# Performance work log

Hardware: AMD Instinct MI355X
Metric: run time of the kernel (lower is better)

Reference implementation:

```python
import jax, jax.numpy as jnp
import numpy as np

NUM_HEADS = 12


def _build_mask(N, unseen_size, dtype):
    # Columns for the last `unseen_size` tokens are masked (-inf) for every
    # query row EXCEPT the diagonal entries in that block (each unseen token
    # may attend to itself). Matches the original Python-loop construction.
    idx = jnp.arange(N)
    col_unseen = idx[None, :] >= (N - unseen_size)
    off_diag = idx[:, None] != idx[None, :]
    return jnp.where(col_unseen & off_diag, -jnp.inf, jnp.asarray(0.0, dtype))


def reference(x, w_qkv, w_proj, b_proj, unseen_size):
    B, N, C = x.shape
    H = NUM_HEADS
    d = C // H
    scale = d ** -0.5
    # qkv: (B,N,3C) -> (3,B,H,N,d)
    qkv = (x @ w_qkv.T).reshape(B, N, 3, H, d).transpose(2, 0, 3, 1, 4)
    q, k, v = qkv[0], qkv[1], qkv[2]
    attn = jnp.einsum('bhqd,bhkd->bhqk', q, k) * scale
    attn = attn + _build_mask(N, unseen_size, attn.dtype)  # broadcast (N,N)
    attn = jax.nn.softmax(attn, axis=-1)
    out = jnp.einsum('bhqk,bhkd->bhqd', attn, v)
    out = out.transpose(0, 2, 1, 3).reshape(B, N, C)
    return out @ w_proj.T + b_proj


def setup_inputs() -> dict:
    key = jax.random.key(0)
    k1, k2, k3 = jax.random.split(key, 3)
    B, N, C = 2, 2048, 768
    x = jax.random.normal(k1, (B, N, C), dtype=jnp.float32)
    w_qkv = jax.random.normal(k2, (3 * C, C), dtype=jnp.float32) * (C ** -0.5)
    w_proj = jax.random.normal(k3, (C, C), dtype=jnp.float32) * (C ** -0.5)
    b_proj = jnp.zeros((C,), dtype=jnp.float32)
    return {"x": x, "w_qkv": w_qkv, "w_proj": w_proj, "b_proj": b_proj,
            "unseen_size": 512}
```

## Files before the change

### kernel.cpp

```cpp
#include <hip/hip_runtime.h>
#include <math.h>

#define NH 12
#define DH 64
#define NSEQ 2048
#define NB 2
#define CDIM 768
#define NVIS 1536

typedef _Float16 half8 __attribute__((ext_vector_type(8)));
typedef _Float16 half4 __attribute__((ext_vector_type(4)));
typedef float floatx4 __attribute__((ext_vector_type(4)));

static constexpr size_t SZ_X    = (size_t)NB*NSEQ*CDIM;
static constexpr size_t SZ_WQKV = (size_t)3*CDIM*CDIM;
static constexpr size_t SZ_WP   = (size_t)CDIM*CDIM;
static constexpr size_t SZ_HEAD = (size_t)NB*NH*NSEQ*DH;

__global__ __launch_bounds__(256) void convert_kernel(
    const float* __restrict__ x, const float* __restrict__ wqkv, const float* __restrict__ wp,
    _Float16* __restrict__ xb, _Float16* __restrict__ wqkvb, _Float16* __restrict__ wpb)
{
  size_t idx = ((size_t)blockIdx.x*256 + threadIdx.x)*4;
  const float* src; _Float16* dst; size_t off;
  if (idx < SZ_X)                        { src = x;    dst = xb;    off = idx; }
  else if (idx < SZ_X+SZ_WQKV)           { src = wqkv; dst = wqkvb; off = idx - SZ_X; }
  else if (idx < SZ_X+SZ_WQKV+SZ_WP)     { src = wp;   dst = wpb;   off = idx - SZ_X - SZ_WQKV; }
  else return;
  float4 v = *reinterpret_cast<const float4*>(src + off);
  _Float16 o[4] = {(_Float16)v.x,(_Float16)v.y,(_Float16)v.z,(_Float16)v.w};
  *reinterpret_cast<uint2*>(dst + off) = *reinterpret_cast<uint2*>(o);
}

template<int MODE>
__global__ __launch_bounds__(256) void gemm_bt(
    const _Float16* __restrict__ A, const _Float16* __restrict__ Bt,
    const float* __restrict__ bias,
    _Float16* __restrict__ qb, _Float16* __restrict__ kb, _Float16* __restrict__ vb,
    float* __restrict__ outp)
{
  constexpr int K = CDIM;
  constexpr int LDSST = 40;
  __shared__ _Float16 As[128*LDSST];
  __shared__ _Float16 Bs[128*LDSST];
  const int tid = threadIdx.x;
  const int lane = tid & 63, wid = tid >> 6;
  const int l15 = lane & 15, quad = lane >> 4;
  const int wm = (wid >> 1)*64, wn = (wid & 1)*64;
  const int tileN = blockIdx.x*128, tileM = blockIdx.y*128;
  const int srow = tid >> 2, scol = (tid & 3)*8;
  floatx4 acc[4][4] = {};
  for (int k0 = 0; k0 < K; k0 += 32) {
    uint4 a0 = *reinterpret_cast<const uint4*>(A  + (size_t)(tileM+srow)*K    + k0 + scol);
    uint4 a1 = *reinterpret_cast<const uint4*>(A  + (size_t)(tileM+64+srow)*K + k0 + scol);
    uint4 b0 = *reinterpret_cast<const uint4*>(Bt + (size_t)(tileN+srow)*K    + k0 + scol);
    uint4 b1 = *reinterpret_cast<const uint4*>(Bt + (size_t)(tileN+64+srow)*K + k0 + scol);
    __syncthreads();
    *reinterpret_cast<uint4*>(&As[srow*LDSST + scol])      = a0;
    *reinterpret_cast<uint4*>(&As[(64+srow)*LDSST + scol]) = a1;
    *reinterpret_cast<uint4*>(&Bs[srow*LDSST + scol])      = b0;
    *reinterpret_cast<uint4*>(&Bs[(64+srow)*LDSST + scol]) = b1;
    __syncthreads();
    half8 af[4], bfr[4];
    #pragma unroll
    for (int mi=0; mi<4; mi++)
      af[mi] = *reinterpret_cast<const half8*>(&As[(wm+mi*16+l15)*LDSST + quad*8]);
    #pragma unroll
    for (int ni=0; ni<4; ni++)
      bfr[ni] = *reinterpret_cast<const half8*>(&Bs[(wn+ni*16+l15)*LDSST + quad*8]);
    #pragma unroll
    for (int mi=0; mi<4; mi++)
      #pragma unroll
      for (int ni=0; ni<4; ni++)
        acc[mi][ni] = __builtin_amdgcn_mfma_f32_16x16x32_f16(af[mi], bfr[ni], acc[mi][ni], 0,0,0);
  }
  #pragma unroll
  for (int mi=0; mi<4; mi++)
    #pragma unroll
    for (int ni=0; ni<4; ni++) {
      int n = tileN + wn + ni*16 + l15;
      int m0 = tileM + wm + mi*16 + quad*4;
      if (MODE == 0) {
        int part = n / CDIM, rem = n - part*CDIM;
        int h = rem >> 6, dd = rem & 63;
        int b = m0 >> 11, i0 = m0 & 2047;
        if (part == 2) {
          half4 pk = {(_Float16)acc[mi][ni][0], (_Float16)acc[mi][ni][1],
                      (_Float16)acc[mi][ni][2], (_Float16)acc[mi][ni][3]};
          *reinterpret_cast<half4*>(&vb[(((size_t)b*NH + h)*DH + dd)*NSEQ + i0]) = pk;
        } else {
          _Float16* dst = part ? kb : qb;
          float sc = part ? 1.0f : 0.125f*1.44269504f;
          #pragma unroll
          for (int r = 0; r < 4; r++)
            dst[(((size_t)b*NH + h)*NSEQ + i0 + r)*DH + dd] = (_Float16)(acc[mi][ni][r]*sc);
        }
      } else {
        #pragma unroll
        for (int r = 0; r < 4; r++)
          outp[(size_t)(m0 + r)*CDIM + n] = acc[mi][ni][r] + bias[n];
      }
    }
}

__global__ __launch_bounds__(256, 3) void fa_kernel(
    const _Float16* __restrict__ qg, const _Float16* __restrict__ kg,
    const _Float16* __restrict__ vtg, _Float16* __restrict__ og)
{
  constexpr int LDP = 72;
  __shared__ _Float16 Ps[64*LDP];
  __shared__ float Ls[4*64];
  const int blk = blockIdx.x;
  const int idx = blk >> 3;
  const int bh = (blk & 7)*3 + (idx % 3);
  const int qbase = (idx / 3) * 64;
  const int tid = threadIdx.x;
  const int lane = tid & 63, w = tid >> 6;
  const int l15 = lane & 15, quad = lane >> 4;
  const _Float16* qp  = qg  + (size_t)bh*NSEQ*DH;
  const _Float16* kbp = kg  + (size_t)bh*NSEQ*DH;
  const _Float16* vbp = vtg + (size_t)bh*DH*NSEQ;
  half8 qf[4][2];
  #pragma unroll
  for (int g = 0; g < 4; g++)
    #pragma unroll
    for (int c = 0; c < 2; c++)
      qf[g][c] = *reinterpret_cast<const half8*>(qp + (size_t)(qbase + g*16 + l15)*DH + c*32 + quad*8);
  const _Float16* kRow = kbp + (size_t)(w*16 + l15)*DH + quad*8;
  const _Float16* vRow = vbp + (size_t)(w*16 + l15)*NSEQ + quad*8;
  half8 kc0 = *reinterpret_cast<const half8*>(kRow);
  half8 kc1 = *reinterpret_cast<const half8*>(kRow + 32);
  half8 vc0 = *reinterpret_cast<const half8*>(vRow);
  half8 vc1 = *reinterpret_cast<const half8*>(vRow + 32);
  floatx4 o[4] = {};
  float lsum[4] = {0.f, 0.f, 0.f, 0.f};
  for (int t = 0; t < 24; t++) {
    const int tn = (t + 1 < 24) ? t + 1 : 0;
    half8 kn0 = *reinterpret_cast<const half8*>(kRow + (size_t)tn*64*DH);
    half8 kn1 = *reinterpret_cast<const half8*>(kRow + (size_t)tn*64*DH + 32);
    half8 vn0 = *reinterpret_cast<const half8*>(vRow + tn*64);
    half8 vn1 = *reinterpret_cast<const half8*>(vRow + tn*64 + 32);
    floatx4 st[4] = {};
    #pragma unroll
    for (int g = 0; g < 4; g++) {
      st[g] = __builtin_amdgcn_mfma_f32_16x16x32_f16(kc0, qf[g][0], st[g], 0,0,0);
      st[g] = __builtin_amdgcn_mfma_f32_16x16x32_f16(kc1, qf[g][1], st[g], 0,0,0);
    }
    half4 pk[4];
    #pragma unroll
    for (int g = 0; g < 4; g++) {
      float e0 = exp2f(st[g][0]), e1 = exp2f(st[g][1]);
      float e2 = exp2f(st[g][2]), e3 = exp2f(st[g][3]);
      lsum[g] += (e0+e1)+(e2+e3);
      pk[g] = half4{(_Float16)e0,(_Float16)e1,(_Float16)e2,(_Float16)e3};
    }
    __syncthreads();
    #pragma unroll
    for (int g = 0; g < 4; g++)
      *reinterpret_cast<half4*>(&Ps[(g*16+l15)*LDP + w*16 + quad*4]) = pk[g];
    __syncthreads();
    #pragma unroll
    for (int g = 0; g < 4; g++) {
      half8 pb0 = *reinterpret_cast<const half8*>(&Ps[(g*16+l15)*LDP + quad*8]);
      half8 pb1 = *reinterpret_cast<const half8*>(&Ps[(g*16+l15)*LDP + 32 + quad*8]);
      o[g] = __builtin_amdgcn_mfma_f32_16x16x32_f16(vc0, pb0, o[g], 0,0,0);
      o[g] = __builtin_amdgcn_mfma_f32_16x16x32_f16(vc1, pb1, o[g], 0,0,0);
    }
    kc0 = kn0; kc1 = kn1; vc0 = vn0; vc1 = vn1;
  }
  #pragma unroll
  for (int g = 0; g < 4; g++) {
    lsum[g] += __shfl_xor(lsum[g], 16);
    lsum[g] += __shfl_xor(lsum[g], 32);
  }
  if (lane < 16) {
    #pragma unroll
    for (int g = 0; g < 4; g++) Ls[w*64 + g*16 + lane] = lsum[g];
  }
  __syncthreads();
  float den[4];
  #pragma unroll
  for (int g = 0; g < 4; g++)
    den[g] = Ls[g*16+l15] + Ls[64+g*16+l15] + Ls[128+g*16+l15] + Ls[192+g*16+l15];
  if (qbase >= NVIS) {
    #pragma unroll
    for (int g = 0; g < 4; g++) {
      half8 kd0 = *reinterpret_cast<const half8*>(kbp + (size_t)(qbase + g*16 + l15)*DH + quad*8);
      half8 kd1 = *reinterpret_cast<const half8*>(kbp + (size_t)(qbase + g*16 + l15)*DH + 32 + quad*8);
      float pd = 0.f;
      #pragma unroll
      for (int j = 0; j < 8; j++)
        pd += (float)qf[g][0][j]*(float)kd0[j] + (float)qf[g][1][j]*(float)kd1[j];
      pd += __shfl_xor(pd, 16);
      pd += __shfl_xor(pd, 32);
      float e = exp2f(pd);
      den[g] += e;
      #pragma unroll
      for (int r = 0; r < 4; r++)
        o[g][r] += e * (float)vbp[(size_t)(w*16+quad*4+r)*NSEQ + qbase + g*16 + l15];
    }
  }
  const int b = bh / NH, h = bh - b*NH;
  #pragma unroll
  for (int g = 0; g < 4; g++) {
    float inv = 1.0f / den[g];
    half4 pk = {(_Float16)(o[g][0]*inv), (_Float16)(o[g][1]*inv),
                (_Float16)(o[g][2]*inv), (_Float16)(o[g][3]*inv)};
    size_t oaddr = ((size_t)b*NSEQ + qbase + g*16 + l15)*CDIM + h*DH + w*16 + quad*4;
    *reinterpret_cast<half4*>(&og[oaddr]) = pk;
  }
}

extern "C" void kernel_launch(void* const* d_in, const int* in_sizes, int n_in,
                              void* d_out, int out_size, void* d_ws, size_t ws_size,
                              hipStream_t stream) {
  (void)in_sizes; (void)n_in; (void)out_size; (void)ws_size;
  const float* x     = (const float*)d_in[0];
  const float* wqkv  = (const float*)d_in[1];
  const float* wproj = (const float*)d_in[2];
  const float* bproj = (const float*)d_in[3];

  _Float16* xb    = (_Float16*)d_ws;
  _Float16* wqkvb = xb + SZ_X;
  _Float16* wpb   = wqkvb + SZ_WQKV;
  _Float16* qb    = wpb + SZ_WP;
  _Float16* kb    = qb + SZ_HEAD;
  _Float16* vb    = kb + SZ_HEAD;
  _Float16* ob    = vb + SZ_HEAD;
  float* outp = (float*)d_out;

  size_t total = SZ_X + SZ_WQKV + SZ_WP;
  int cblocks = (int)((total/4 + 255)/256);
  convert_kernel<<<cblocks, 256, 0, stream>>>(x, wqkv, wproj, xb, wqkvb, wpb);
  gemm_bt<0><<<dim3(3*CDIM/128, NB*NSEQ/128), 256, 0, stream>>>(xb, wqkvb, nullptr, qb, kb, vb, nullptr);
  fa_kernel<<<NB*NH*(NSEQ/64), 256, 0, stream>>>(qb, kb, vb, ob);
  gemm_bt<1><<<dim3(CDIM/128, NB*NSEQ/128), 256, 0, stream>>>(ob, wpb, bproj, nullptr, nullptr, nullptr, outp);
}
```

Before: 176.4 us.

## Use direct global-to-LDS loads with swizzle in GEMM, widen attention KV tile

The GEMM now stages A/B tiles with global_load_lds (direct global-to-LDS DMA) into an XOR-swizzled unpadded layout instead of going through registers. The projection GEMM gets a narrower 64-column tile so more blocks are launched. The attention kernel processes 128 keys per iteration instead of 64, which halves the number of barrier pairs and doubles the register prefetch depth for K and V. It also swaps exp2f for the builtin exp2. Risks include higher register pressure in the attention kernel and correctness depending on the swizzle matching the LDS write pattern.

```diff
diff --git a/kernel.cpp b/kernel.cpp
--- a/kernel.cpp
+++ b/kernel.cpp
@@ -16,6 +16,10 @@
 static constexpr size_t SZ_WQKV = (size_t)3*CDIM*CDIM;
 static constexpr size_t SZ_WP   = (size_t)CDIM*CDIM;
 static constexpr size_t SZ_HEAD = (size_t)NB*NH*NSEQ*DH;
+
+#define GLOAD_LDS16(gp, lp) \
+  __builtin_amdgcn_global_load_lds((const __attribute__((address_space(1))) void*)(gp), \
+                                   (__attribute__((address_space(3))) void*)(lp), 16, 0, 0)
 
 __global__ __launch_bounds__(256) void convert_kernel(
     const float* __restrict__ x, const float* __restrict__ wqkv, const float* __restrict__ wp,
@@ -32,7 +36,7 @@
   *reinterpret_cast<uint2*>(dst + off) = *reinterpret_cast<uint2*>(o);
 }
 
-template<int MODE>
+template<int MODE, int BN>
 __global__ __launch_bounds__(256) void gemm_bt(
     const _Float16* __restrict__ A, const _Float16* __restrict__ Bt,
     const float* __restrict__ bias,
@@ -40,44 +44,53 @@
     float* __restrict__ outp)
 {
   constexpr int K = CDIM;
-  constexpr int LDSST = 40;
-  __shared__ _Float16 As[128*LDSST];
-  __shared__ _Float16 Bs[128*LDSST];
+  constexpr int BM = 128, BK = 32;
+  constexpr int MI = (BN == 128) ? 4 : 2;
+  constexpr int NI = 4;
+  __shared__ _Float16 As[BM*BK];
+  __shared__ _Float16 Bs[BN*BK];
   const int tid = threadIdx.x;
   const int lane = tid & 63, wid = tid >> 6;
   const int l15 = lane & 15, quad = lane >> 4;
-  const int wm = (wid >> 1)*64, wn = (wid & 1)*64;
-  const int tileN = blockIdx.x*128, tileM = blockIdx.y*128;
-  const int srow = tid >> 2, scol = (tid & 3)*8;
-  floatx4 acc[4][4] = {};
-  for (int k0 = 0; k0 < K; k0 += 32) {
-    uint4 a0 = *reinterpret_cast<const uint4*>(A  + (size_t)(tileM+srow)*K    + k0 + scol);
-    uint4 a1 = *reinterpret_cast<const uint4*>(A  + (size_t)(tileM+64+srow)*K + k0 + scol);
-    uint4 b0 = *reinterpret_cast<const uint4*>(Bt + (size_t)(tileN+srow)*K    + k0 + scol);
-    uint4 b1 = *reinterpret_cast<const uint4*>(Bt + (size_t)(tileN+64+srow)*K + k0 + scol);
-    __syncthreads();
-    *reinterpret_cast<uint4*>(&As[srow*LDSST + scol])      = a0;
-    *reinterpret_cast<uint4*>(&As[(64+srow)*LDSST + scol]) = a1;
-    *reinterpret_cast<uint4*>(&Bs[srow*LDSST + scol])      = b0;
-    *reinterpret_cast<uint4*>(&Bs[(64+srow)*LDSST + scol]) = b1;
-    __syncthreads();
-    half8 af[4], bfr[4];
-    #pragma unroll
-    for (int mi=0; mi<4; mi++)
-      af[mi] = *reinterpret_cast<const half8*>(&As[(wm+mi*16+l15)*LDSST + quad*8]);
-    #pragma unroll
-    for (int ni=0; ni<4; ni++)
-      bfr[ni] = *reinterpret_cast<const half8*>(&Bs[(wn+ni*16+l15)*LDSST + quad*8]);
-    #pragma unroll
-    for (int mi=0; mi<4; mi++)
-      #pragma unroll
-      for (int ni=0; ni<4; ni++)
+  const int wm = (BN == 128) ? (wid >> 1)*64 : wid*32;
+  const int wn = (BN == 128) ? (wid & 1)*64 : 0;
+  const int tileN = blockIdx.x*BN, tileM = blockIdx.y*BM;
+  const int lrow = lane >> 2, lchunk = lane & 3;
+  const int gcol = ((lchunk ^ (lrow >> 1)) & 3)*8;
+  const _Float16* gA0 = A  + (size_t)(tileM + wid*32      + lrow)*K + gcol;
+  const _Float16* gA1 = A  + (size_t)(tileM + wid*32 + 16 + lrow)*K + gcol;
+  const _Float16* gB0 = Bt + (size_t)(tileN + ((BN==128) ? wid*32 : wid*16) + lrow)*K + gcol;
+  const _Float16* gB1 = Bt + (size_t)(tileN + wid*32 + 16 + lrow)*K + gcol;
+  _Float16* lA0 = As + (wid*32)*BK;
+  _Float16* lA1 = As + (wid*32 + 16)*BK;
+  _Float16* lB0 = Bs + ((BN==128) ? wid*32 : wid*16)*BK;
+  _Float16* lB1 = Bs + (wid*32 + 16)*BK;
+  const int cp = ((quad ^ (l15 >> 1)) & 3)*8;
+  floatx4 acc[MI][NI] = {};
+  for (int k0 = 0; k0 < K; k0 += BK) {
+    __syncthreads();
+    GLOAD_LDS16(gA0 + k0, lA0);
+    GLOAD_LDS16(gA1 + k0, lA1);
+    GLOAD_LDS16(gB0 + k0, lB0);
+    if (BN == 128) GLOAD_LDS16(gB1 + k0, lB1);
+    __syncthreads();
+    half8 af[MI], bfr[NI];
+    #pragma unroll
+    for (int mi = 0; mi < MI; mi++)
+      af[mi] = *reinterpret_cast<const half8*>(&As[(wm + mi*16 + l15)*BK + cp]);
+    #pragma unroll
+    for (int ni = 0; ni < NI; ni++)
+      bfr[ni] = *reinterpret_cast<const half8*>(&Bs[(wn + ni*16 + l15)*BK + cp]);
+    #pragma unroll
+    for (int mi = 0; mi < MI; mi++)
+      #pragma unroll
+      for (int ni = 0; ni < NI; ni++)
         acc[mi][ni] = __builtin_amdgcn_mfma_f32_16x16x32_f16(af[mi], bfr[ni], acc[mi][ni], 0,0,0);
   }
   #pragma unroll
-  for (int mi=0; mi<4; mi++)
-    #pragma unroll
-    for (int ni=0; ni<4; ni++) {
+  for (int mi = 0; mi < MI; mi++)
+    #pragma unroll
+    for (int ni = 0; ni < NI; ni++) {
       int n = tileN + wn + ni*16 + l15;
       int m0 = tileM + wm + mi*16 + quad*4;
       if (MODE == 0) {
@@ -107,7 +120,7 @@
     const _Float16* __restrict__ qg, const _Float16* __restrict__ kg,
     const _Float16* __restrict__ vtg, _Float16* __restrict__ og)
 {
-  constexpr int LDP = 72;
+  constexpr int LDP = 136;
   __shared__ _Float16 Ps[64*LDP];
   __shared__ float Ls[4*64];
   const int blk = blockIdx.x;
@@ -128,45 +141,64 @@
       qf[g][c] = *reinterpret_cast<const half8*>(qp + (size_t)(qbase + g*16 + l15)*DH + c*32 + quad*8);
   const _Float16* kRow = kbp + (size_t)(w*16 + l15)*DH + quad*8;
   const _Float16* vRow = vbp + (size_t)(w*16 + l15)*NSEQ + quad*8;
-  half8 kc0 = *reinterpret_cast<const half8*>(kRow);
-  half8 kc1 = *reinterpret_cast<const half8*>(kRow + 32);
-  half8 vc0 = *reinterpret_cast<const half8*>(vRow);
-  half8 vc1 = *reinterpret_cast<const half8*>(vRow + 32);
+  half8 kc[2][2], vc[2][2];
+  #pragma unroll
+  for (int s = 0; s < 2; s++)
+    #pragma unroll
+    for (int c = 0; c < 2; c++) {
+      kc[s][c] = *reinterpret_cast<const half8*>(kRow + (size_t)(s*64)*DH + c*32);
+      vc[s][c] = *reinterpret_cast<const half8*>(vRow + s*64 + c*32);
+    }
   floatx4 o[4] = {};
   float lsum[4] = {0.f, 0.f, 0.f, 0.f};
-  for (int t = 0; t < 24; t++) {
-    const int tn = (t + 1 < 24) ? t + 1 : 0;
-    half8 kn0 = *reinterpret_cast<const half8*>(kRow + (size_t)tn*64*DH);
-    half8 kn1 = *reinterpret_cast<const half8*>(kRow + (size_t)tn*64*DH + 32);
-    half8 vn0 = *reinterpret_cast<const half8*>(vRow + tn*64);
-    half8 vn1 = *reinterpret_cast<const half8*>(vRow + tn*64 + 32);
-    floatx4 st[4] = {};
+  for (int t = 0; t < 12; t++) {
+    const int tn = (t + 1 < 12) ? t + 1 : 0;
+    half8 kn[2][2], vn[2][2];
+    #pragma unroll
+    for (int s = 0; s < 2; s++)
+      #pragma unroll
+      for (int c = 0; c < 2; c++) {
+        kn[s][c] = *reinterpret_cast<const half8*>(kRow + (size_t)(tn*128 + s*64)*DH + c*32);
+        vn[s][c] = *reinterpret_cast<const half8*>(vRow + tn*128 + s*64 + c*32);
+      }
+    half4 pk[2][4];
+    #pragma unroll
+    for (int s = 0; s < 2; s++) {
+      floatx4 st[4] = {};
+      #pragma unroll
+      for (int g = 0; g < 4; g++) {
+        st[g] = __builtin_amdgcn_mfma_f32_16x16x32_f16(kc[s][0], qf[g][0], st[g], 0,0,0);
+        st[g] = __builtin_amdgcn_mfma_f32_16x16x32_f16(kc[s][1], qf[g][1], st[g], 0,0,0);
+      }
+      #pragma unroll
+      for (int g = 0; g < 4; g++) {
+        float e0 = __builtin_exp2f(st[g][0]), e1 = __builtin_exp2f(st[g][1]);
+        float e2 = __builtin_exp2f(st[g][2]), e3 = __builtin_exp2f(st[g][3]);
+        lsum[g] += (e0+e1)+(e2+e3);
+        pk[s][g] = half4{(_Float16)e0,(_Float16)e1,(_Float16)e2,(_Float16)e3};
+      }
+    }
+    __syncthreads();
+    #pragma unroll
+    for (int s = 0; s < 2; s++)
+      #pragma unroll
+      for (int g = 0; g < 4; g++)
+        *reinterpret_cast<half4*>(&Ps[(g*16+l15)*LDP + s*64 + w*16 + quad*4]) = pk[s][g];
+    __syncthreads();
     #pragma unroll
     for (int g = 0; g < 4; g++) {
-      st[g] = __builtin_amdgcn_mfma_f32_16x16x32_f16(kc0, qf[g][0], st[g], 0,0,0);
-      st[g] = __builtin_amdgcn_mfma_f32_16x16x32_f16(kc1, qf[g][1], st[g], 0,0,0);
-    }
-    half4 pk[4];
-    #pragma unroll
-    for (int g = 0; g < 4; g++) {
-      float e0 = exp2f(st[g][0]), e1 = exp2f(st[g][1]);
-      float e2 = exp2f(st[g][2]), e3 = exp2f(st[g][3]);
-      lsum[g] += (e0+e1)+(e2+e3);
-      pk[g] = half4{(_Float16)e0,(_Float16)e1,(_Float16)e2,(_Float16)e3};
-    }
-    __syncthreads();
-    #pragma unroll
-    for (int g = 0; g < 4; g++)
-      *reinterpret_cast<half4*>(&Ps[(g*16+l15)*LDP + w*16 + quad*4]) = pk[g];
-    __syncthreads();
-    #pragma unroll
-    for (int g = 0; g < 4; g++) {
-      half8 pb0 = *reinterpret_cast<const half8*>(&Ps[(g*16+l15)*LDP + quad*8]);
-      half8 pb1 = *reinterpret_cast<const half8*>(&Ps[(g*16+l15)*LDP + 32 + quad*8]);
-      o[g] = __builtin_amdgcn_mfma_f32_16x16x32_f16(vc0, pb0, o[g], 0,0,0);
-      o[g] = __builtin_amdgcn_mfma_f32_16x16x32_f16(vc1, pb1, o[g], 0,0,0);
-    }
-    kc0 = kn0; kc1 = kn1; vc0 = vn0; vc1 = vn1;
+      #pragma unroll
+      for (int s = 0; s < 2; s++)
+        #pragma unroll
+        for (int c = 0; c < 2; c++) {
+          half8 pb = *reinterpret_cast<const half8*>(&Ps[(g*16+l15)*LDP + s*64 + c*32 + quad*8]);
+          o[g] = __builtin_amdgcn_mfma_f32_16x16x32_f16(vc[s][c], pb, o[g], 0,0,0);
+        }
+    }
+    #pragma unroll
+    for (int s = 0; s < 2; s++)
+      #pragma unroll
+      for (int c = 0; c < 2; c++) { kc[s][c] = kn[s][c]; vc[s][c] = vn[s][c]; }
   }
   #pragma unroll
   for (int g = 0; g < 4; g++) {
@@ -193,7 +225,7 @@
         pd += (float)qf[g][0][j]*(float)kd0[j] + (float)qf[g][1][j]*(float)kd1[j];
       pd += __shfl_xor(pd, 16);
       pd += __shfl_xor(pd, 32);
-      float e = exp2f(pd);
+      float e = __builtin_exp2f(pd);
       den[g] += e;
       #pragma unroll
       for (int r = 0; r < 4; r++)
@@ -232,7 +264,7 @@
   size_t total = SZ_X + SZ_WQKV + SZ_WP;
   int cblocks = (int)((total/4 + 255)/256);
   convert_kernel<<<cblocks, 256, 0, stream>>>(x, wqkv, wproj, xb, wqkvb, wpb);
-  gemm_bt<0><<<dim3(3*CDIM/128, NB*NSEQ/128), 256, 0, stream>>>(xb, wqkvb, nullptr, qb, kb, vb, nullptr);
+  gemm_bt<0,128><<<dim3(3*CDIM/128, NB*NSEQ/128), 256, 0, stream>>>(xb, wqkvb, nullptr, qb, kb, vb, nullptr);
   fa_kernel<<<NB*NH*(NSEQ/64), 256, 0, stream>>>(qb, kb, vb, ob);
-  gemm_bt<1><<<dim3(CDIM/128, NB*NSEQ/128), 256, 0, stream>>>(ob, wpb, bproj, nullptr, nullptr, nullptr, outp);
-}
+  gemm_bt<1,64><<<dim3(CDIM/64, NB*NSEQ/128), 256, 0, stream>>>(ob, wpb, bproj, nullptr, nullptr, nullptr, outp);
+}
```

Result: faster. 166.0 us (-5.9%).
